# Kernel tuning notes

Hardware: AMD Instinct MI355X
Metric: run time of the kernel (lower is better)

The kernel has to match this reference:

```python
import jax, jax.numpy as jnp
import numpy as np

B, F, V, D = 16384, 16, 100000, 16  # batch, n_fields, vocab, embed_dim; dims = F*D = 256
EPS = 1e-5


def _bn(x, g, b):
    # torch.nn.BatchNorm1d in training mode: biased batch variance
    m = x.mean(0)
    v = x.var(0)
    return g * (x - m) * jax.lax.rsqrt(v + EPS) + b


def setup_inputs() -> dict:
    ks = iter(jax.random.split(jax.random.key(0), 40))

    def rn(shape, s=0.05):
        return jax.random.normal(next(ks), shape, jnp.float32) * s

    return {
        "feat_ids": jax.random.randint(next(ks), (B, F), 0, V, jnp.int32),
        "domain_ids": jax.random.randint(next(ks), (B,), 0, 3, jnp.int32),
        "emb": rn((F, V, D), 0.1),
        "hW0": rn((256, 128)), "hb0": jnp.zeros(128), "hg0": jnp.ones(128), "hbe0": jnp.zeros(128),
        "hW1": rn((128, 64)), "hb1": jnp.zeros(64), "hg1": jnp.ones(64), "hbe1": jnp.zeros(64),
        "hW2": rn((64, 1024)), "hb2": jnp.zeros(1024), "hg2": jnp.ones(1024), "hbe2": jnp.zeros(1024),
        "cw": rn((3, 256)), "cb": jnp.zeros((3, 256)),
        "mW0": rn((256, 512)), "mb0": jnp.zeros(512), "mg0": jnp.ones(512), "mbe0": jnp.zeros(512),
        "mW1": rn((512, 256)), "mb1": jnp.zeros(256), "mg1": jnp.ones(256), "mbe1": jnp.zeros(256),
        "u0": rn((256, 32)), "u1": rn((32, 32)), "v0": rn((32, 32)), "v1": rn((32, 256)),
        "ab0": jnp.zeros(32), "ab1": jnp.zeros(256),
        "gamma1": jnp.ones(256), "bias1": jnp.zeros(256),
        "lw": rn((512,)), "lb": jnp.zeros(1),
    }


def _forward(feat_ids, emb, hW0, hb0, hg0, hbe0, hW1, hb1, hg1, hbe1,
             hW2, hb2, hg2, hbe2, cw, cb, mW0, mb0, mg0, mbe0,
             mW1, mb1, mg1, mbe1, u0, u1, v0, v1, ab0, ab1,
             gamma1, bias1, lw, lb):
    b, f = feat_ids.shape
    # EmbeddingLayer(squeeze_dim=True): per-field lookup then concat -> [B, F*D]
    e = emb[jnp.arange(f)[None, :], feat_ids].reshape(b, -1)
    h = e
    for W, bb, g, be in ((hW0, hb0, hg0, hbe0), (hW1, hb1, hg1, hbe1), (hW2, hb2, hg2, hbe2)):
        h = jax.nn.relu(_bn(h @ W + bb, g, be))
    k = u1.shape[0]
    H = h.reshape(b, k, k)  # [B, k, k]
    # CrossNetwork: x_{l+1} = x0 * (x_l . w_l) + b_l + x_l
    x = e
    for i in range(cw.shape[0]):
        x = e * (x @ cw[i])[:, None] + cb[i] + x
    cn_out = x  # [B, 256]
    m = e
    for W, bb, g, be in ((mW0, mb0, mg0, mbe0), (mW1, mb1, mg1, mbe1)):
        m = jax.nn.relu(_bn(m @ W + bb, g, be))
    # hyper low-rank adapter: einsum('mi,bij,jn->bmn') applied lazily so the
    # [B,256,32] per-sample weight is never materialized (associativity)
    t = jax.nn.sigmoid(jnp.einsum('bi,bij->bj', m @ u0, H) @ v0 + ab0)   # [B, 32]
    t = jnp.einsum('bi,bij->bj', t @ u1, H) @ v1 + ab1                    # [B, 256]
    mu = t.mean(0)
    var = t.var(0, ddof=1)  # torch.var default is unbiased
    m = gamma1 * (t - mu) / jnp.sqrt(var + EPS) + bias1 + m  # norm + residual
    y = jnp.concatenate([cn_out, m], axis=1) @ lw + lb[0]     # LR head
    # Every domain branch computes identical values (shared weights, full-batch
    # input, dropout p=0), so the torch.where domain-select is the identity.
    return jax.nn.sigmoid(y)  # [B]


def reference(feat_ids, domain_ids, emb, hW0, hb0, hg0, hbe0, hW1, hb1, hg1, hbe1,
              hW2, hb2, hg2, hbe2, cw, cb, mW0, mb0, mg0, mbe0,
              mW1, mb1, mg1, mbe1, u0, u1, v0, v1, ab0, ab1,
              gamma1, bias1, lw, lb):
    return _forward(feat_ids, emb, hW0, hb0, hg0, hbe0, hW1, hb1, hg1, hbe1,
                    hW2, hb2, hg2, hbe2, cw, cb, mW0, mb0, mg0, mbe0,
                    mW1, mb1, mg1, mbe1, u0, u1, v0, v1, ab0, ab1,
                    gamma1, bias1, lw, lb)
```

## Files before the change

kernel.cpp:

```cpp
#include <hip/hip_runtime.h>

typedef unsigned short u16;
typedef __attribute__((ext_vector_type(8))) short bf16x8;
typedef __attribute__((ext_vector_type(4))) float f32x4;
#define BATCH 16384

__device__ __forceinline__ float b2f(u16 u){ unsigned int i=((unsigned int)u)<<16; float f; __builtin_memcpy(&f,&i,4); return f; }
__device__ __forceinline__ u16 f2b(float f){ unsigned int x; __builtin_memcpy(&x,&f,4); unsigned int r=(x + 0x7fffu + ((x>>16)&1u))>>16; return (u16)r; }

__global__ __launch_bounds__(256) void prep_kernel(float* __restrict__ S,
                                                   const float* __restrict__ w0, const float* __restrict__ w1,
                                                   const float* __restrict__ w2, const float* __restrict__ w3,
                                                   const float* __restrict__ w4, const float* __restrict__ w5,
                                                   const float* __restrict__ w6,
                                                   u16* __restrict__ t0, u16* __restrict__ t1,
                                                   u16* __restrict__ t2, u16* __restrict__ t3,
                                                   u16* __restrict__ t4, u16* __restrict__ t5,
                                                   u16* __restrict__ t6,
                                                   const int* __restrict__ ids,
                                                   const float* __restrict__ emb,
                                                   u16* __restrict__ e){
  int blk = blockIdx.x;
  if (blk < 48){
    int i = blk*256 + threadIdx.x;
    if (i < 12288) S[i] = 0.f;
  } else if (blk < 1552){
    int b = blk - 48;
    if (b < 128){        int idx=(b-0)*256+threadIdx.x;    t0[idx]=f2b(w0[(idx%256)*128  + idx/256]); }
    else if (b < 160){   int idx=(b-128)*256+threadIdx.x;  t1[idx]=f2b(w1[(idx%128)*64   + idx/128]); }
    else if (b < 416){   int idx=(b-160)*256+threadIdx.x;  t2[idx]=f2b(w2[(idx%64)*1024  + idx/64]);  }
    else if (b < 928){   int idx=(b-416)*256+threadIdx.x;  t3[idx]=f2b(w3[(idx%256)*512  + idx/256]); }
    else if (b < 1440){  int idx=(b-928)*256+threadIdx.x;  t4[idx]=f2b(w4[(idx%512)*256  + idx/512]); }
    else if (b < 1472){  int idx=(b-1440)*256+threadIdx.x; t5[idx]=f2b(w5[(idx%256)*32   + idx/256]); }
    else {               int idx=(b-1472)*256+threadIdx.x; t6[idx]=f2b(w6[(idx%32)*256   + idx/32]);  }
  } else {
    int b = blk - 1552;
    int tid = threadIdx.x;
    int f = tid >> 4, d = tid & 15;
    int id = ids[b*16 + f];
    e[(size_t)b*256 + tid] = f2b(emb[((size_t)f*100000 + (size_t)id)*16 + d]);
  }
}

#define ASTR 40
__global__ __launch_bounds__(256) void gemm_mfma(const u16* __restrict__ A,
                                                 const u16* __restrict__ Wt,
                                                 const float* __restrict__ bias,
                                                 u16* __restrict__ C,
                                                 const float* __restrict__ asums,
                                                 const float* __restrict__ asumsq,
                                                 const float* __restrict__ ag,
                                                 const float* __restrict__ abe,
                                                 float* __restrict__ sums,
                                                 float* __restrict__ sumsq,
                                                 int N, int K){
  __shared__ u16 lds[64*ASTR*2];
  __shared__ float bnS[512], bnB[512];
  u16* As = lds;
  u16* Bs = lds + 64*ASTR;
  int tid = threadIdx.x;
  int n0 = blockIdx.x*64, m0 = blockIdx.y*64;
  int srow = tid >> 2, skoff = (tid & 3)*8;
  int lane = tid & 63, w = tid >> 6, quad = lane >> 4, m16 = lane & 15;
  if (asums != nullptr){
    for (int k = tid; k < K; k += 256){
      float mean = asums[k] * (1.f/(float)BATCH);
      float var  = asumsq[k] * (1.f/(float)BATCH) - mean*mean;
      float sc   = ag[k] * rsqrtf(var + 1e-5f);
      bnS[k] = sc;
      bnB[k] = abe[k] - mean*sc;
    }
    __syncthreads();
  }
  f32x4 acc[4] = {};
  int ng = n0 + srow;
  for (int k0 = 0; k0 < K; k0 += 32){
    uint4 av = *(const uint4*)(A + (size_t)(m0+srow)*K + k0 + skoff);
    u16 at[8]; __builtin_memcpy(at, &av, 16);
    if (asums != nullptr){
#pragma unroll
      for (int j=0;j<8;j++){
        float v = b2f(at[j]) * bnS[k0+skoff+j] + bnB[k0+skoff+j];
        at[j] = f2b(v > 0.f ? v : 0.f);
      }
    }
    __builtin_memcpy(&av, at, 16);
    *(uint4*)&As[srow*ASTR + skoff] = av;
    uint4 wv = make_uint4(0u,0u,0u,0u);
    if (ng < N) wv = *(const uint4*)(Wt + (size_t)ng*K + k0 + skoff);
    *(uint4*)&Bs[srow*ASTR + skoff] = wv;
    __syncthreads();
    bf16x8 bfrag = *(bf16x8*)&Bs[(w*16 + m16)*ASTR + quad*8];
#pragma unroll
    for (int mc=0;mc<4;mc++){
      bf16x8 afrag = *(bf16x8*)&As[(mc*16 + m16)*ASTR + quad*8];
      acc[mc] = __builtin_amdgcn_mfma_f32_16x16x32_bf16(afrag, bfrag, acc[mc], 0, 0, 0);
    }
    __syncthreads();
  }
  int cw = n0 + w*16 + m16;
  float bv = (bias != nullptr && cw < N) ? bias[cw] : 0.f;
  float cs = 0.f, cq = 0.f;
  u16* Cs = lds;
#pragma unroll
  for (int mc=0;mc<4;mc++)
#pragma unroll
    for (int r=0;r<4;r++){
      float v = acc[mc][r] + bv;
      cs += v; cq += v*v;
      Cs[(mc*16 + quad*4 + r)*72 + w*16 + m16] = f2b(v);
    }
  if (sums != nullptr){
    cs += __shfl_xor(cs, 16, 64); cs += __shfl_xor(cs, 32, 64);
    cq += __shfl_xor(cq, 16, 64); cq += __shfl_xor(cq, 32, 64);
    if (quad == 0 && cw < N){ atomicAdd(&sums[cw], cs); atomicAdd(&sumsq[cw], cq); }
  }
  __syncthreads();
  int row = tid >> 2, c4 = (tid & 3)*16;
  int cg = n0 + c4;
  if (cg < N){
    uint4 p0 = *(uint4*)&Cs[row*72 + c4];
    uint4 p1 = *(uint4*)&Cs[row*72 + c4 + 8];
    *(uint4*)(C + (size_t)(m0+row)*N + cg) = p0;
    *(uint4*)(C + (size_t)(m0+row)*N + cg + 8) = p1;
  }
}

__global__ __launch_bounds__(256) void adapter_core(const u16* __restrict__ H,
                                                    const u16* __restrict__ P,
                                                    const float* __restrict__ v0,
                                                    const float* __restrict__ u1,
                                                    const float* __restrict__ ab0,
                                                    const float* __restrict__ hsums,
                                                    const float* __restrict__ hsumsq,
                                                    const float* __restrict__ hg,
                                                    const float* __restrict__ hbe,
                                                    u16* __restrict__ Z2){
  __shared__ __align__(16) u16 Hs[8*1024];
  __shared__ float bnS[1024], bnB[1024];
  __shared__ float v0s[1024], u1s[1024];
  __shared__ float Ps[256], qs[256], t1s[256], ss[256];
  __shared__ float ab0s[32];
  int tid = threadIdx.x;
  int r = tid >> 5, j = tid & 31;
  size_t row0 = (size_t)blockIdx.x * 8;

  for (int k = tid; k < 1024; k += 256){
    float mean = hsums[k] * (1.f/(float)BATCH);
    float var  = hsumsq[k] * (1.f/(float)BATCH) - mean*mean;
    float sc   = hg[k] * rsqrtf(var + 1e-5f);
    bnS[k] = sc;
    bnB[k] = hbe[k] - mean*sc;
    v0s[k] = v0[k]; u1s[k] = u1[k];
  }
  if (tid < 32) ab0s[tid] = ab0[tid];
  Ps[tid] = b2f(P[row0*32 + tid]);
  __syncthreads();
  for (int k = tid; k < 8*1024; k += 256){
    int col = k & 1023;
    float v = b2f(H[row0*1024 + k]) * bnS[col] + bnB[col];
    Hs[k] = f2b(v > 0.f ? v : 0.f);
  }
  __syncthreads();

  float acc = 0.f;
#pragma unroll
  for (int i=0;i<32;i++) acc += Ps[r*32+i] * b2f(Hs[r*1024 + i*32 + j]);
  qs[r*32+j] = acc;
  __syncthreads();

  acc = ab0s[j];
#pragma unroll
  for (int i=0;i<32;i++) acc += qs[r*32+i] * v0s[i*32+j];
  t1s[r*32+j] = 1.f / (1.f + __expf(-acc));
  __syncthreads();

  acc = 0.f;
#pragma unroll
  for (int i=0;i<32;i++) acc += t1s[r*32+i] * u1s[i*32+j];
  ss[r*32+j] = acc;
  __syncthreads();

  acc = 0.f;
#pragma unroll
  for (int i=0;i<32;i++) acc += ss[r*32+i] * b2f(Hs[r*1024 + i*32 + j]);
  Z2[(row0 + r)*32 + j] = f2b(acc);
}

__global__ __launch_bounds__(256) void final_kernel(const u16* __restrict__ e,
                                                    const float* __restrict__ cw,
                                                    const float* __restrict__ cb,
                                                    const u16* __restrict__ t,
                                                    const u16* __restrict__ mo,
                                                    const float* __restrict__ tsums,
                                                    const float* __restrict__ tsumsq,
                                                    const float* __restrict__ tg,
                                                    const float* __restrict__ tbe,
                                                    const float* __restrict__ msums,
                                                    const float* __restrict__ msumsq,
                                                    const float* __restrict__ mg,
                                                    const float* __restrict__ mbe,
                                                    const float* __restrict__ lw,
                                                    const float* __restrict__ lb,
                                                    float* __restrict__ out){
  __shared__ float tS[256], tB[256], mS[256], mB[256];
  int tid = threadIdx.x;
  {
    int c = tid;
    float mean = tsums[c] * (1.f/(float)BATCH);
    float var  = (tsumsq[c] - mean*mean*(float)BATCH) * (1.f/(float)(BATCH-1));
    float sc   = tg[c] * rsqrtf(var + 1e-5f);
    tS[c] = sc; tB[c] = tbe[c] - mean*sc;
    float mmean = msums[c] * (1.f/(float)BATCH);
    float mvar  = msumsq[c] * (1.f/(float)BATCH) - mmean*mmean;
    float msc   = mg[c] * rsqrtf(mvar + 1e-5f);
    mS[c] = msc; mB[c] = mbe[c] - mmean*msc;
  }
  __syncthreads();
  int wave = tid >> 6, lane = tid & 63;
  int b = blockIdx.x*4 + wave;
  int n4 = lane*4;
  ushort4 ev = *(const ushort4*)(e + (size_t)b*256 + n4);
  float ec[4] = { b2f(ev.x), b2f(ev.y), b2f(ev.z), b2f(ev.w) };
  float x[4]  = { ec[0], ec[1], ec[2], ec[3] };
  for (int i=0;i<3;i++){
    float p = 0.f;
#pragma unroll
    for (int q=0;q<4;q++) p += x[q] * cw[i*256 + n4 + q];
#pragma unroll
    for (int o=1;o<64;o<<=1) p += __shfl_xor(p, o, 64);
#pragma unroll
    for (int q=0;q<4;q++) x[q] = ec[q]*p + cb[i*256 + n4 + q] + x[q];
  }
  ushort4 tv = *(const ushort4*)(t  + (size_t)b*256 + n4);
  ushort4 mv = *(const ushort4*)(mo + (size_t)b*256 + n4);
  float ta[4] = { b2f(tv.x), b2f(tv.y), b2f(tv.z), b2f(tv.w) };
  float ma[4] = { b2f(mv.x), b2f(mv.y), b2f(mv.z), b2f(mv.w) };
  float p = 0.f;
#pragma unroll
  for (int q=0;q<4;q++){
    int n = n4 + q;
    p += x[q] * lw[n];
    float mr = ma[q]*mS[n] + mB[n];
    mr = mr > 0.f ? mr : 0.f;
    float mf = tS[n]*ta[q] + tB[n] + mr;
    p += mf * lw[256 + n];
  }
#pragma unroll
  for (int o=32;o>0;o>>=1) p += __shfl_down(p, o, 64);
  if (lane == 0){
    float y = p + lb[0];
    out[b] = 1.f / (1.f + __expf(-y));
  }
}

extern "C" void kernel_launch(void* const* d_in, const int* in_sizes, int n_in,
                              void* d_out, int out_size, void* d_ws, size_t ws_size,
                              hipStream_t stream) {
  const int B = BATCH;
  const int*   feat = (const int*)d_in[0];
  const float* emb  = (const float*)d_in[2];
  const float* hW0 = (const float*)d_in[3],  *hb0 = (const float*)d_in[4],  *hg0 = (const float*)d_in[5],  *hbe0 = (const float*)d_in[6];
  const float* hW1 = (const float*)d_in[7],  *hb1 = (const float*)d_in[8],  *hg1 = (const float*)d_in[9],  *hbe1 = (const float*)d_in[10];
  const float* hW2 = (const float*)d_in[11], *hb2 = (const float*)d_in[12], *hg2 = (const float*)d_in[13], *hbe2 = (const float*)d_in[14];
  const float* cw  = (const float*)d_in[15], *cb  = (const float*)d_in[16];
  const float* mW0 = (const float*)d_in[17], *mb0 = (const float*)d_in[18], *mg0 = (const float*)d_in[19], *mbe0 = (const float*)d_in[20];
  const float* mW1 = (const float*)d_in[21], *mb1 = (const float*)d_in[22], *mg1 = (const float*)d_in[23], *mbe1 = (const float*)d_in[24];
  const float* u0  = (const float*)d_in[25], *u1  = (const float*)d_in[26];
  const float* v0  = (const float*)d_in[27], *v1  = (const float*)d_in[28];
  const float* ab0 = (const float*)d_in[29], *ab1 = (const float*)d_in[30];
  const float* gamma1 = (const float*)d_in[31], *bias1 = (const float*)d_in[32];
  const float* lw  = (const float*)d_in[33], *lb = (const float*)d_in[34];
  float* out = (float*)d_out;

  char* base = (char*)d_ws;
  const size_t MB = 1024*1024;
  u16* H    = (u16*)(base);
  u16* e    = (u16*)(base + 32*MB);
  u16* Y0   = (u16*)(base + 40*MB);
  u16* Y1   = (u16*)(base + 44*MB);
  u16* M0   = (u16*)(base + 40*MB);
  u16* T    = (u16*)(base + 40*MB);
  u16* P    = (u16*)(base + 48*MB);
  u16* Z2   = (u16*)(base + 49*MB);
  u16* Mout = (u16*)(base + 56*MB);
  u16* hW0t = (u16*)(base + 56*MB);
  u16* hW1t = hW0t + 32768;
  u16* hW2t = hW1t + 8192;
  u16* mW0t = hW2t + 65536;
  float* S  = (float*)(base + 64*MB);
  auto sums  = [&](int l){ return S + l*2048; };
  auto sumsq = [&](int l){ return S + l*2048 + 1024; };
  u16* mW1t = (u16*)(base + 64*MB + 64*1024);
  u16* u0t  = mW1t + 131072;
  u16* v1t  = u0t + 8192;

  prep_kernel<<<17936, 256, 0, stream>>>(S, hW0, hW1, hW2, mW0, mW1, u0, v1,
                                         hW0t, hW1t, hW2t, mW0t, mW1t, u0t, v1t,
                                         feat, emb, e);

  gemm_mfma<<<dim3(2, B/64), 256, 0, stream>>>(e,  hW0t, hb0, Y0,
      nullptr, nullptr, nullptr, nullptr, sums(0), sumsq(0), 128, 256);
  gemm_mfma<<<dim3(1, B/64), 256, 0, stream>>>(Y0, hW1t, hb1, Y1,
      sums(0), sumsq(0), hg0, hbe0, sums(1), sumsq(1), 64, 128);
  gemm_mfma<<<dim3(16, B/64), 256, 0, stream>>>(Y1, hW2t, hb2, H,
      sums(1), sumsq(1), hg1, hbe1, sums(2), sumsq(2), 1024, 64);

  gemm_mfma<<<dim3(8, B/64), 256, 0, stream>>>(e,  mW0t, mb0, M0,
      nullptr, nullptr, nullptr, nullptr, sums(3), sumsq(3), 512, 256);
  gemm_mfma<<<dim3(4, B/64), 256, 0, stream>>>(M0, mW1t, mb1, Mout,
      sums(3), sumsq(3), mg0, mbe0, sums(4), sumsq(4), 256, 512);

  gemm_mfma<<<dim3(1, B/64), 256, 0, stream>>>(Mout, u0t, nullptr, P,
      sums(4), sumsq(4), mg1, mbe1, nullptr, nullptr, 32, 256);
  adapter_core<<<B/8, 256, 0, stream>>>(H, P, v0, u1, ab0,
      sums(2), sumsq(2), hg2, hbe2, Z2);
  gemm_mfma<<<dim3(4, B/64), 256, 0, stream>>>(Z2, v1t, ab1, T,
      nullptr, nullptr, nullptr, nullptr, sums(5), sumsq(5), 256, 32);

  final_kernel<<<B/4, 256, 0, stream>>>(e, cw, cb, T, Mout,
      sums(5), sumsq(5), gamma1, bias1,
      sums(4), sumsq(4), mg1, mbe1, lw, lb, out);
}
```

Baseline: 357.1 us.

## Fuse both first-layer GEMMs, fold P projection into adapter, vectorize embedding gather

```diff
diff --git a/kernel.cpp b/kernel.cpp
--- a/kernel.cpp
+++ b/kernel.cpp
@@ -9,36 +9,45 @@
 __device__ __forceinline__ u16 f2b(float f){ unsigned int x; __builtin_memcpy(&x,&f,4); unsigned int r=(x + 0x7fffu + ((x>>16)&1u))>>16; return (u16)r; }
 
 __global__ __launch_bounds__(256) void prep_kernel(float* __restrict__ S,
+                                                   const float* __restrict__ hb0, const float* __restrict__ mb0,
+                                                   float* __restrict__ catb,
                                                    const float* __restrict__ w0, const float* __restrict__ w1,
                                                    const float* __restrict__ w2, const float* __restrict__ w3,
                                                    const float* __restrict__ w4, const float* __restrict__ w5,
                                                    const float* __restrict__ w6,
-                                                   u16* __restrict__ t0, u16* __restrict__ t1,
-                                                   u16* __restrict__ t2, u16* __restrict__ t3,
-                                                   u16* __restrict__ t4, u16* __restrict__ t5,
-                                                   u16* __restrict__ t6,
+                                                   u16* __restrict__ catWt, u16* __restrict__ t1,
+                                                   u16* __restrict__ t2, u16* __restrict__ t4,
+                                                   u16* __restrict__ t5, u16* __restrict__ t6,
                                                    const int* __restrict__ ids,
                                                    const float* __restrict__ emb,
                                                    u16* __restrict__ e){
   int blk = blockIdx.x;
-  if (blk < 48){
-    int i = blk*256 + threadIdx.x;
-    if (i < 12288) S[i] = 0.f;
-  } else if (blk < 1552){
-    int b = blk - 48;
-    if (b < 128){        int idx=(b-0)*256+threadIdx.x;    t0[idx]=f2b(w0[(idx%256)*128  + idx/256]); }
-    else if (b < 160){   int idx=(b-128)*256+threadIdx.x;  t1[idx]=f2b(w1[(idx%128)*64   + idx/128]); }
-    else if (b < 416){   int idx=(b-160)*256+threadIdx.x;  t2[idx]=f2b(w2[(idx%64)*1024  + idx/64]);  }
-    else if (b < 928){   int idx=(b-416)*256+threadIdx.x;  t3[idx]=f2b(w3[(idx%256)*512  + idx/256]); }
-    else if (b < 1440){  int idx=(b-928)*256+threadIdx.x;  t4[idx]=f2b(w4[(idx%512)*256  + idx/512]); }
-    else if (b < 1472){  int idx=(b-1440)*256+threadIdx.x; t5[idx]=f2b(w5[(idx%256)*32   + idx/256]); }
-    else {               int idx=(b-1472)*256+threadIdx.x; t6[idx]=f2b(w6[(idx%32)*256   + idx/32]);  }
+  int tid = threadIdx.x;
+  if (blk < 18){
+    int i = blk*256 + tid;
+    if (i < 4480) S[i] = 0.f;
+  } else if (blk == 18){
+    for (int i = tid; i < 640; i += 256) catb[i] = (i < 128) ? hb0[i] : mb0[i-128];
+  } else if (blk < 1523){
+    int c = blk - 19;
+    if (c < 640){        int idx=c*256+tid;        int n=idx>>8, k=idx&255;
+                         catWt[idx] = f2b(n<128 ? w0[k*128+n] : w3[k*512+(n-128)]); }
+    else if (c < 672){   int idx=(c-640)*256+tid;  t1[idx]=f2b(w1[(idx%128)*64   + idx/128]); }
+    else if (c < 928){   int idx=(c-672)*256+tid;  t2[idx]=f2b(w2[(idx%64)*1024  + idx/64]);  }
+    else if (c < 1440){  int idx=(c-928)*256+tid;  t4[idx]=f2b(w4[(idx%512)*256  + idx/512]); }
+    else if (c < 1472){  int idx=(c-1440)*256+tid; t5[idx]=f2b(w5[(idx%256)*32   + idx/256]); }
+    else {               int idx=(c-1472)*256+tid; t6[idx]=f2b(w6[(idx%32)*256   + idx/32]);  }
   } else {
-    int b = blk - 1552;
-    int tid = threadIdx.x;
-    int f = tid >> 4, d = tid & 15;
+    int g = blk - 1523;
+    int b = g*16 + (tid >> 4), f = tid & 15;
     int id = ids[b*16 + f];
-    e[(size_t)b*256 + tid] = f2b(emb[((size_t)f*100000 + (size_t)id)*16 + d]);
+    const float4* src = (const float4*)(emb + ((size_t)f*100000 + (size_t)id)*16);
+    float4 v0 = src[0], v1 = src[1], v2 = src[2], v3 = src[3];
+    u16 o[16] = { f2b(v0.x),f2b(v0.y),f2b(v0.z),f2b(v0.w), f2b(v1.x),f2b(v1.y),f2b(v1.z),f2b(v1.w),
+                  f2b(v2.x),f2b(v2.y),f2b(v2.z),f2b(v2.w), f2b(v3.x),f2b(v3.y),f2b(v3.z),f2b(v3.w) };
+    uint4 p0, p1; __builtin_memcpy(&p0, &o[0], 16); __builtin_memcpy(&p1, &o[8], 16);
+    uint4* dst = (uint4*)(e + (size_t)b*256 + f*16);
+    dst[0] = p0; dst[1] = p1;
   }
 }
 
@@ -46,7 +55,9 @@
 __global__ __launch_bounds__(256) void gemm_mfma(const u16* __restrict__ A,
                                                  const u16* __restrict__ Wt,
                                                  const float* __restrict__ bias,
-                                                 u16* __restrict__ C,
+                                                 u16* __restrict__ Ca,
+                                                 u16* __restrict__ Cb,
+                                                 int Nsplit,
                                                  const float* __restrict__ asums,
                                                  const float* __restrict__ asumsq,
                                                  const float* __restrict__ ag,
@@ -119,15 +130,20 @@
   int row = tid >> 2, c4 = (tid & 3)*16;
   int cg = n0 + c4;
   if (cg < N){
+    u16* outp; int stride, colbase;
+    if (Cb != nullptr && n0 >= Nsplit){ outp = Cb; stride = N - Nsplit; colbase = cg - Nsplit; }
+    else if (Cb != nullptr){            outp = Ca; stride = Nsplit;     colbase = cg; }
+    else {                              outp = Ca; stride = N;          colbase = cg; }
     uint4 p0 = *(uint4*)&Cs[row*72 + c4];
     uint4 p1 = *(uint4*)&Cs[row*72 + c4 + 8];
-    *(uint4*)(C + (size_t)(m0+row)*N + cg) = p0;
-    *(uint4*)(C + (size_t)(m0+row)*N + cg + 8) = p1;
+    *(uint4*)(outp + (size_t)(m0+row)*stride + colbase) = p0;
+    *(uint4*)(outp + (size_t)(m0+row)*stride + colbase + 8) = p1;
   }
 }
 
 __global__ __launch_bounds__(256) void adapter_core(const u16* __restrict__ H,
-                                                    const u16* __restrict__ P,
+                                                    const u16* __restrict__ Mout,
+                                                    const u16* __restrict__ u0t,
                                                     const float* __restrict__ v0,
                                                     const float* __restrict__ u1,
                                                     const float* __restrict__ ab0,
@@ -135,10 +151,16 @@
                                                     const float* __restrict__ hsumsq,
                                                     const float* __restrict__ hg,
                                                     const float* __restrict__ hbe,
+                                                    const float* __restrict__ msums,
+                                                    const float* __restrict__ msumsq,
+                                                    const float* __restrict__ mg,
+                                                    const float* __restrict__ mbe,
                                                     u16* __restrict__ Z2){
-  __shared__ __align__(16) u16 Hs[8*1024];
+  __shared__ __align__(16) u16 big[8192];
   __shared__ float bnS[1024], bnB[1024];
-  __shared__ float v0s[1024], u1s[1024];
+  __shared__ u16 v0s[1024], u1s[1024];
+  __shared__ float mS[256], mB[256];
+  __shared__ __align__(16) u16 aS[2048];
   __shared__ float Ps[256], qs[256], t1s[256], ss[256];
   __shared__ float ab0s[32];
   int tid = threadIdx.x;
@@ -149,41 +171,62 @@
     float mean = hsums[k] * (1.f/(float)BATCH);
     float var  = hsumsq[k] * (1.f/(float)BATCH) - mean*mean;
     float sc   = hg[k] * rsqrtf(var + 1e-5f);
-    bnS[k] = sc;
-    bnB[k] = hbe[k] - mean*sc;
-    v0s[k] = v0[k]; u1s[k] = u1[k];
-  }
+    bnS[k] = sc; bnB[k] = hbe[k] - mean*sc;
+    v0s[k] = f2b(v0[k]); u1s[k] = f2b(u1[k]);
+  }
+  {
+    int c = tid;
+    float mean = msums[c] * (1.f/(float)BATCH);
+    float var  = msumsq[c] * (1.f/(float)BATCH) - mean*mean;
+    float sc   = mg[c] * rsqrtf(var + 1e-5f);
+    mS[c] = sc; mB[c] = mbe[c] - mean*sc;
+  }
+  for (int k = tid; k < 8192; k += 256) big[k] = u0t[k];
+  for (int k = tid; k < 2048; k += 256) aS[k] = Mout[row0*256 + k];
   if (tid < 32) ab0s[tid] = ab0[tid];
-  Ps[tid] = b2f(P[row0*32 + tid]);
-  __syncthreads();
-  for (int k = tid; k < 8*1024; k += 256){
+  __syncthreads();
+  for (int k = tid; k < 2048; k += 256){
+    int col = k & 255;
+    float v = b2f(aS[k]) * mS[col] + mB[col];
+    aS[k] = f2b(v > 0.f ? v : 0.f);
+  }
+  __syncthreads();
+  {
+    float acc = 0.f;
+    for (int k8 = 0; k8 < 256; k8 += 8){
+      uint4 va; __builtin_memcpy(&va, &aS[r*256 + k8], 16);
+      uint4 vu; __builtin_memcpy(&vu, &big[j*256 + k8], 16);
+      u16 ta[8], tu[8]; __builtin_memcpy(ta, &va, 16); __builtin_memcpy(tu, &vu, 16);
+#pragma unroll
+      for (int q=0;q<8;q++) acc += b2f(ta[q]) * b2f(tu[q]);
+    }
+    Ps[tid] = acc;
+  }
+  __syncthreads();
+  for (int k = tid; k < 8192; k += 256){
     int col = k & 1023;
     float v = b2f(H[row0*1024 + k]) * bnS[col] + bnB[col];
-    Hs[k] = f2b(v > 0.f ? v : 0.f);
-  }
-  __syncthreads();
-
+    big[k] = f2b(v > 0.f ? v : 0.f);
+  }
+  __syncthreads();
   float acc = 0.f;
 #pragma unroll
-  for (int i=0;i<32;i++) acc += Ps[r*32+i] * b2f(Hs[r*1024 + i*32 + j]);
-  qs[r*32+j] = acc;
-  __syncthreads();
-
+  for (int i=0;i<32;i++) acc += Ps[r*32+i] * b2f(big[r*1024 + i*32 + j]);
+  qs[tid] = acc;
+  __syncthreads();
   acc = ab0s[j];
 #pragma unroll
-  for (int i=0;i<32;i++) acc += qs[r*32+i] * v0s[i*32+j];
-  t1s[r*32+j] = 1.f / (1.f + __expf(-acc));
-  __syncthreads();
-
+  for (int i=0;i<32;i++) acc += qs[r*32+i] * b2f(v0s[i*32+j]);
+  t1s[tid] = 1.f / (1.f + __expf(-acc));
+  __syncthreads();
   acc = 0.f;
 #pragma unroll
-  for (int i=0;i<32;i++) acc += t1s[r*32+i] * u1s[i*32+j];
-  ss[r*32+j] = acc;
-  __syncthreads();
-
+  for (int i=0;i<32;i++) acc += t1s[r*32+i] * b2f(u1s[i*32+j]);
+  ss[tid] = acc;
+  __syncthreads();
   acc = 0.f;
 #pragma unroll
-  for (int i=0;i<32;i++) acc += ss[r*32+i] * b2f(Hs[r*1024 + i*32 + j]);
+  for (int i=0;i<32;i++) acc += ss[r*32+i] * b2f(big[r*1024 + i*32 + j]);
   Z2[(row0 + r)*32 + j] = f2b(acc);
 }
 
@@ -279,46 +322,41 @@
   u16* e    = (u16*)(base + 32*MB);
   u16* Y0   = (u16*)(base + 40*MB);
   u16* Y1   = (u16*)(base + 44*MB);
-  u16* M0   = (u16*)(base + 40*MB);
-  u16* T    = (u16*)(base + 40*MB);
-  u16* P    = (u16*)(base + 48*MB);
-  u16* Z2   = (u16*)(base + 49*MB);
-  u16* Mout = (u16*)(base + 56*MB);
-  u16* hW0t = (u16*)(base + 56*MB);
-  u16* hW1t = hW0t + 32768;
+  u16* M0   = (u16*)(base + 48*MB);
+  u16* Mout = (u16*)(base + 64*MB);
+  u16* T    = (u16*)(base + 72*MB);
+  u16* Z2   = (u16*)(base + 80*MB);
+  u16* catWt= (u16*)(base + 88*MB);
+  u16* hW1t = catWt + 163840;
   u16* hW2t = hW1t + 8192;
-  u16* mW0t = hW2t + 65536;
-  float* S  = (float*)(base + 64*MB);
-  auto sums  = [&](int l){ return S + l*2048; };
-  auto sumsq = [&](int l){ return S + l*2048 + 1024; };
-  u16* mW1t = (u16*)(base + 64*MB + 64*1024);
+  u16* mW1t = hW2t + 65536;
   u16* u0t  = mW1t + 131072;
   u16* v1t  = u0t + 8192;
-
-  prep_kernel<<<17936, 256, 0, stream>>>(S, hW0, hW1, hW2, mW0, mW1, u0, v1,
-                                         hW0t, hW1t, hW2t, mW0t, mW1t, u0t, v1t,
-                                         feat, emb, e);
-
-  gemm_mfma<<<dim3(2, B/64), 256, 0, stream>>>(e,  hW0t, hb0, Y0,
-      nullptr, nullptr, nullptr, nullptr, sums(0), sumsq(0), 128, 256);
-  gemm_mfma<<<dim3(1, B/64), 256, 0, stream>>>(Y0, hW1t, hb1, Y1,
-      sums(0), sumsq(0), hg0, hbe0, sums(1), sumsq(1), 64, 128);
-  gemm_mfma<<<dim3(16, B/64), 256, 0, stream>>>(Y1, hW2t, hb2, H,
-      sums(1), sumsq(1), hg1, hbe1, sums(2), sumsq(2), 1024, 64);
-
-  gemm_mfma<<<dim3(8, B/64), 256, 0, stream>>>(e,  mW0t, mb0, M0,
-      nullptr, nullptr, nullptr, nullptr, sums(3), sumsq(3), 512, 256);
-  gemm_mfma<<<dim3(4, B/64), 256, 0, stream>>>(M0, mW1t, mb1, Mout,
-      sums(3), sumsq(3), mg0, mbe0, sums(4), sumsq(4), 256, 512);
-
-  gemm_mfma<<<dim3(1, B/64), 256, 0, stream>>>(Mout, u0t, nullptr, P,
-      sums(4), sumsq(4), mg1, mbe1, nullptr, nullptr, 32, 256);
-  adapter_core<<<B/8, 256, 0, stream>>>(H, P, v0, u1, ab0,
-      sums(2), sumsq(2), hg2, hbe2, Z2);
-  gemm_mfma<<<dim3(4, B/64), 256, 0, stream>>>(Z2, v1t, ab1, T,
-      nullptr, nullptr, nullptr, nullptr, sums(5), sumsq(5), 256, 32);
+  float* catb = (float*)(v1t + 8192);
+  float* S    = catb + 640;
+
+  prep_kernel<<<2547, 256, 0, stream>>>(S, hb0, mb0, catb,
+                                        hW0, hW1, hW2, mW0, mW1, u0, v1,
+                                        catWt, hW1t, hW2t, mW1t, u0t, v1t,
+                                        feat, emb, e);
+
+  gemm_mfma<<<dim3(10, B/64), 256, 0, stream>>>(e, catWt, catb, Y0, M0, 128,
+      nullptr, nullptr, nullptr, nullptr, S+0, S+640, 640, 256);
+
+  gemm_mfma<<<dim3(1, B/64), 256, 0, stream>>>(Y0, hW1t, hb1, Y1, nullptr, 0,
+      S+0, S+640, hg0, hbe0, S+1280, S+1344, 64, 128);
+  gemm_mfma<<<dim3(16, B/64), 256, 0, stream>>>(Y1, hW2t, hb2, H, nullptr, 0,
+      S+1280, S+1344, hg1, hbe1, S+1408, S+2432, 1024, 64);
+
+  gemm_mfma<<<dim3(4, B/64), 256, 0, stream>>>(M0, mW1t, mb1, Mout, nullptr, 0,
+      S+128, S+768, mg0, mbe0, S+3456, S+3712, 256, 512);
+
+  adapter_core<<<B/8, 256, 0, stream>>>(H, Mout, u0t, v0, u1, ab0,
+      S+1408, S+2432, hg2, hbe2, S+3456, S+3712, mg1, mbe1, Z2);
+  gemm_mfma<<<dim3(4, B/64), 256, 0, stream>>>(Z2, v1t, ab1, T, nullptr, 0,
+      nullptr, nullptr, nullptr, nullptr, S+3968, S+4224, 256, 32);
 
   final_kernel<<<B/4, 256, 0, stream>>>(e, cw, cb, T, Mout,
-      sums(5), sumsq(5), gamma1, bias1,
-      sums(4), sumsq(4), mg1, mbe1, lw, lb, out);
-}
+      S+3968, S+4224, gamma1, bias1,
+      S+3456, S+3712, mg1, mbe1, lw, lb, out);
+}
```

Measured after the change: 369.4 us. 3.5% more time.
